# Kernel tuning notes

Measured on AMD Instinct MI355X. Metric: run time of the kernel, lower is better.

## Reference

```python
import jax, jax.numpy as jnp
import numpy as np

P = 16  # patch size
D = 768  # embedding dim


def setup_inputs() -> dict:
    key = jax.random.key(0)
    k_img, k_w, k_b = jax.random.split(key, 3)
    B, H, W, C = 64, 224, 224, 3
    image = jax.random.normal(k_img, (B, H, W, C), dtype=jnp.float32)
    patch_dim = P * P * C  # 768
    # Keras Dense default: glorot_uniform kernel, zeros bias
    limit = np.sqrt(6.0 / (patch_dim + D)).astype(np.float32)
    W_proj = jax.random.uniform(k_w, (patch_dim, D), dtype=jnp.float32,
                                minval=-limit, maxval=limit)
    b_proj = jnp.zeros((D,), dtype=jnp.float32)
    return {"image": image, "W_proj": W_proj, "b_proj": b_proj}


def reference(image, W_proj, b_proj):
    B, H, W, C = image.shape
    nh, nw = H // P, W // P
    # Fused im2col replacing the per-patch slicing loop:
    # [B,H,W,C] -> [B, nh, P, nw, P, C] -> [B, nh, nw, P, P, C] -> [B, nh*nw, P*P*C]
    # Row-major (p_i, p_j) patch order matches the original nested loop, and
    # flatten of a [B,P,P,C] slice matches the (P,P,C) raveling here.
    patches = image.reshape(B, nh, P, nw, P, C)
    patches = patches.transpose(0, 1, 3, 2, 4, 5).reshape(B, nh * nw, P * P * C)
    # Dense + exact GELU (tf.keras.activations.gelu default approximate=False)
    x = jnp.einsum('bnp,pd->bnd', patches, W_proj) + b_proj
    return jax.nn.gelu(x, approximate=False)
```

## Files before the change

kernel.cpp:

```cpp
#include <hip/hip_runtime.h>
#include <hip/hip_bf16.h>
#include <math.h>

#define MM 12544
#define KK 768
#define NN 768
#define BM 64
#define BN 256
#define BK 64
#define KT 12
#define MT 196
#define NT 3
#define TILE_B_BYTES (BN*BK*2)

#define WTPACK_BLOCKS ((NN * 96) / 256)

typedef __bf16 v8bf __attribute__((ext_vector_type(8)));
typedef float  v4f  __attribute__((ext_vector_type(4)));

__global__ __launch_bounds__(256) void wpack_kernel(const float* __restrict__ w,
                                                    __hip_bfloat16* __restrict__ wpack) {
    int tid = blockIdx.x * 256 + threadIdx.x;
    int n   = tid % 768;
    int gg  = tid / 768;
    int k0  = gg * 8;
    float f[8];
#pragma unroll
    for (int j = 0; j < 8; j++) f[j] = w[(size_t)(k0 + j) * NN + n];
    int nt = n >> 8;
    int nr = n & 255;
    int kt = gg >> 3;
    int g  = gg & 7;
    int gs = g ^ (nr & 7);
    union { __hip_bfloat16 h[8]; uint4 u; } o;
#pragma unroll
    for (int j = 0; j < 8; j++) o.h[j] = __float2bfloat16(f[j]);
    *(uint4*)(wpack + ((size_t)(nt * KT + kt) * BN + nr) * BK + gs * 8) = o.u;
}

__device__ __forceinline__ float gelu_fast(float x) {
    float t2 = 1.5957691216057308f * x * (1.0f + 0.044715f * x * x);
    float e  = __expf(t2);
    float r  = __builtin_amdgcn_rcpf(e + 1.0f);
    return x - x * r;
}

__global__ __launch_bounds__(256, 3) void gemm_fused(const float* __restrict__ img,
                                                     const __hip_bfloat16* __restrict__ wpack,
                                                     const float* __restrict__ bias,
                                                     float* __restrict__ out) {
    __shared__ __align__(16) __hip_bfloat16 As[BM * BK];
    __shared__ __align__(16) __hip_bfloat16 Bs[BN * BK];

    const int blk = blockIdx.x;
    const int nt  = blk % 3;
    const int mt  = blk / 3;

    const int tid  = threadIdx.x;
    const int lane = tid & 63;
    const int wave = tid >> 6;
    const int wn   = wave * 64;
    const int col  = lane & 15;
    const int quad = lane >> 4;
    const int cl7  = col & 7;

    const int r  = tid >> 2;
    const int c  = tid & 3;
    const int m  = mt * BM + r;
    const int b  = m / 196;
    const int pm = m - b * 196;
    const int pr = pm / 14;
    const int pc = pm - pr * 14;
    const float* abase = img + (size_t)((b * 224 + pr * 16) * 224 + pc * 16) * 3;
    int rem = (c == 3) ? 0 : c * 16;
    const float* asrc = abase + ((c == 3) ? 672 : 0) + rem;
    const int s0 = (2 * c) ^ (r & 7);
    uint4* aw0 = (uint4*)(As + r * BK + s0 * 8);
    uint4* aw1 = (uint4*)(As + r * BK + (s0 ^ 1) * 8);

    v4f acc[4][4];
    const v4f vzero = {0.f, 0.f, 0.f, 0.f};
#pragma unroll
    for (int a = 0; a < 4; a++)
#pragma unroll
        for (int cc = 0; cc < 4; cc++) acc[a][cc] = vzero;

    const char* bT = (const char*)wpack + (size_t)nt * KT * TILE_B_BYTES;

    float4 a0, a1, a2, a3;
    {
        const float4* ap = (const float4*)asrc;
        a0 = ap[0]; a1 = ap[1]; a2 = ap[2]; a3 = ap[3];
        asrc += (rem < 32) ? 688 : 1312;
        rem   = (rem < 32) ? rem + 16 : 0;
    }

    for (int kt = 0; kt < KT; kt++) {
#pragma unroll
        for (int p = 0; p < 8; p++) {
            int off = p * 4096 + tid * 16;
            __builtin_amdgcn_global_load_lds(
                (const __attribute__((address_space(1))) void*)(bT + off),
                (__attribute__((address_space(3))) void*)((char*)Bs + off), 16, 0, 0);
        }
        bT += TILE_B_BYTES;

        union { __hip_bfloat16 h[8]; uint4 u; } o0, o1;
        o0.h[0] = __float2bfloat16(a0.x); o0.h[1] = __float2bfloat16(a0.y);
        o0.h[2] = __float2bfloat16(a0.z); o0.h[3] = __float2bfloat16(a0.w);
        o0.h[4] = __float2bfloat16(a1.x); o0.h[5] = __float2bfloat16(a1.y);
        o0.h[6] = __float2bfloat16(a1.z); o0.h[7] = __float2bfloat16(a1.w);
        o1.h[0] = __float2bfloat16(a2.x); o1.h[1] = __float2bfloat16(a2.y);
        o1.h[2] = __float2bfloat16(a2.z); o1.h[3] = __float2bfloat16(a2.w);
        o1.h[4] = __float2bfloat16(a3.x); o1.h[5] = __float2bfloat16(a3.y);
        o1.h[6] = __float2bfloat16(a3.z); o1.h[7] = __float2bfloat16(a3.w);
        *aw0 = o0.u;
        *aw1 = o1.u;

        if (kt + 1 < KT) {
            const float4* ap = (const float4*)asrc;
            a0 = ap[0]; a1 = ap[1]; a2 = ap[2]; a3 = ap[3];
            asrc += (rem < 32) ? 688 : 1312;
            rem   = (rem < 32) ? rem + 16 : 0;
        }
        __syncthreads();

#pragma unroll
        for (int ks = 0; ks < 2; ks++) {
            const int gs = (ks * 4 + quad) ^ cl7;
            const v8bf* pa = (const v8bf*)(As + col * BK + gs * 8);
            const v8bf* pb = (const v8bf*)(Bs + (wn + col) * BK + gs * 8);
            v8bf af[4], bfr[4];
#pragma unroll
            for (int mi = 0; mi < 4; mi++) af[mi] = pa[mi * 128];
#pragma unroll
            for (int ni = 0; ni < 4; ni++) bfr[ni] = pb[ni * 128];
#pragma unroll
            for (int mi = 0; mi < 4; mi++)
#pragma unroll
                for (int ni = 0; ni < 4; ni++)
                    acc[mi][ni] = __builtin_amdgcn_mfma_f32_16x16x32_bf16(
                        af[mi], bfr[ni], acc[mi][ni], 0, 0, 0);
        }
        __syncthreads();
    }

#pragma unroll
    for (int ni = 0; ni < 4; ni++) {
        int n    = nt * BN + wn + ni * 16 + col;
        float bv = bias[n];
#pragma unroll
        for (int mi = 0; mi < 4; mi++) {
            int rowb = mt * BM + mi * 16 + quad * 4;
            float* po = out + (size_t)rowb * NN + n;
#pragma unroll
            for (int rg = 0; rg < 4; rg++) {
                float x = acc[mi][ni][rg] + bv;
                po[(size_t)rg * NN] = gelu_fast(x);
            }
        }
    }
}

extern "C" void kernel_launch(void* const* d_in, const int* in_sizes, int n_in,
                              void* d_out, int out_size, void* d_ws, size_t ws_size,
                              hipStream_t stream) {
    const float* img   = (const float*)d_in[0];
    const float* wproj = (const float*)d_in[1];
    const float* bias  = (const float*)d_in[2];
    float* out = (float*)d_out;

    __hip_bfloat16* wpack = (__hip_bfloat16*)d_ws;

    wpack_kernel<<<dim3(WTPACK_BLOCKS), dim3(256), 0, stream>>>(wproj, wpack);
    gemm_fused<<<dim3(MT * NT), dim3(256), 0, stream>>>(img, wpack, bias, out);
}
```

Measured before the change: 123.4 us.

## Double-buffer LDS tiles and remap blocks per XCD for L2 locality

```diff
diff --git a/kernel.cpp b/kernel.cpp
--- a/kernel.cpp
+++ b/kernel.cpp
@@ -45,16 +45,19 @@
     return x - x * r;
 }
 
-__global__ __launch_bounds__(256, 3) void gemm_fused(const float* __restrict__ img,
+__global__ __launch_bounds__(256, 2) void gemm_fused(const float* __restrict__ img,
                                                      const __hip_bfloat16* __restrict__ wpack,
                                                      const float* __restrict__ bias,
                                                      float* __restrict__ out) {
-    __shared__ __align__(16) __hip_bfloat16 As[BM * BK];
-    __shared__ __align__(16) __hip_bfloat16 Bs[BN * BK];
+    __shared__ __align__(16) __hip_bfloat16 As[2][BM * BK];
+    __shared__ __align__(16) __hip_bfloat16 Bs[2][BN * BK];
 
-    const int blk = blockIdx.x;
-    const int nt  = blk % 3;
-    const int mt  = blk / 3;
+    const int h   = blockIdx.x;
+    const int xcd = h & 7;
+    const int j   = h >> 3;
+    const int u   = (xcd < 4 ? xcd * 74 : 296 + (xcd - 4) * 73) + j;
+    const int nt  = u % 3;
+    const int mt  = u / 3;
 
     const int tid  = threadIdx.x;
     const int lane = tid & 63;
@@ -74,9 +77,9 @@
     const float* abase = img + (size_t)((b * 224 + pr * 16) * 224 + pc * 16) * 3;
     int rem = (c == 3) ? 0 : c * 16;
     const float* asrc = abase + ((c == 3) ? 672 : 0) + rem;
-    const int s0 = (2 * c) ^ (r & 7);
-    uint4* aw0 = (uint4*)(As + r * BK + s0 * 8);
-    uint4* aw1 = (uint4*)(As + r * BK + (s0 ^ 1) * 8);
+    const int s0   = (2 * c) ^ (r & 7);
+    const int aoff0 = r * BK + s0 * 8;
+    const int aoff1 = r * BK + (s0 ^ 1) * 8;
 
     v4f acc[4][4];
     const v4f vzero = {0.f, 0.f, 0.f, 0.f};
@@ -87,63 +90,72 @@
 
     const char* bT = (const char*)wpack + (size_t)nt * KT * TILE_B_BYTES;
 
+#define LOAD_A_REGS()                                            \
+    {   const float4* ap = (const float4*)asrc;                  \
+        a0 = ap[0]; a1 = ap[1]; a2 = ap[2]; a3 = ap[3];          \
+        asrc += (rem < 32) ? 688 : 1312;                         \
+        rem   = (rem < 32) ? rem + 16 : 0;  }
+
+#define STAGE_B(buf)                                                          \
+    {   _Pragma("unroll")                                                     \
+        for (int p = 0; p < 8; p++) {                                         \
+            int off = p * 4096 + tid * 16;                                    \
+            __builtin_amdgcn_global_load_lds(                                 \
+                (const __attribute__((address_space(1))) void*)(bT + off),    \
+                (__attribute__((address_space(3))) void*)((char*)Bs[buf] + off), \
+                16, 0, 0);                                                    \
+        }                                                                     \
+        bT += TILE_B_BYTES;  }
+
+#define WRITE_A(buf)                                                          \
+    {   union { __hip_bfloat16 hh[8]; uint4 uu; } o0, o1;                     \
+        o0.hh[0] = __float2bfloat16(a0.x); o0.hh[1] = __float2bfloat16(a0.y); \
+        o0.hh[2] = __float2bfloat16(a0.z); o0.hh[3] = __float2bfloat16(a0.w); \
+        o0.hh[4] = __float2bfloat16(a1.x); o0.hh[5] = __float2bfloat16(a1.y); \
+        o0.hh[6] = __float2bfloat16(a1.z); o0.hh[7] = __float2bfloat16(a1.w); \
+        o1.hh[0] = __float2bfloat16(a2.x); o1.hh[1] = __float2bfloat16(a2.y); \
+        o1.hh[2] = __float2bfloat16(a2.z); o1.hh[3] = __float2bfloat16(a2.w); \
+        o1.hh[4] = __float2bfloat16(a3.x); o1.hh[5] = __float2bfloat16(a3.y); \
+        o1.hh[6] = __float2bfloat16(a3.z); o1.hh[7] = __float2bfloat16(a3.w); \
+        *(uint4*)(As[buf] + aoff0) = o0.uu;                                   \
+        *(uint4*)(As[buf] + aoff1) = o1.uu;  }
+
+#define COMPUTE(buf)                                                          \
+    {   _Pragma("unroll")                                                     \
+        for (int ks = 0; ks < 2; ks++) {                                      \
+            const int gs = (ks * 4 + quad) ^ cl7;                             \
+            const v8bf* pa = (const v8bf*)(As[buf] + col * BK + gs * 8);      \
+            const v8bf* pb = (const v8bf*)(Bs[buf] + (wn + col) * BK + gs * 8);\
+            v8bf af[4], bfr[4];                                               \
+            _Pragma("unroll")                                                 \
+            for (int mi = 0; mi < 4; mi++) af[mi] = pa[mi * 128];             \
+            _Pragma("unroll")                                                 \
+            for (int ni = 0; ni < 4; ni++) bfr[ni] = pb[ni * 128];            \
+            _Pragma("unroll")                                                 \
+            for (int mi = 0; mi < 4; mi++)                                    \
+                _Pragma("unroll")                                             \
+                for (int ni = 0; ni < 4; ni++)                                \
+                    acc[mi][ni] = __builtin_amdgcn_mfma_f32_16x16x32_bf16(    \
+                        af[mi], bfr[ni], acc[mi][ni], 0, 0, 0);               \
+        }  }
+
     float4 a0, a1, a2, a3;
-    {
-        const float4* ap = (const float4*)asrc;
-        a0 = ap[0]; a1 = ap[1]; a2 = ap[2]; a3 = ap[3];
-        asrc += (rem < 32) ? 688 : 1312;
-        rem   = (rem < 32) ? rem + 16 : 0;
-    }
-
-    for (int kt = 0; kt < KT; kt++) {
-#pragma unroll
-        for (int p = 0; p < 8; p++) {
-            int off = p * 4096 + tid * 16;
-            __builtin_amdgcn_global_load_lds(
-                (const __attribute__((address_space(1))) void*)(bT + off),
-                (__attribute__((address_space(3))) void*)((char*)Bs + off), 16, 0, 0);
-        }
-        bT += TILE_B_BYTES;
-
-        union { __hip_bfloat16 h[8]; uint4 u; } o0, o1;
-        o0.h[0] = __float2bfloat16(a0.x); o0.h[1] = __float2bfloat16(a0.y);
-        o0.h[2] = __float2bfloat16(a0.z); o0.h[3] = __float2bfloat16(a0.w);
-        o0.h[4] = __float2bfloat16(a1.x); o0.h[5] = __float2bfloat16(a1.y);
-        o0.h[6] = __float2bfloat16(a1.z); o0.h[7] = __float2bfloat16(a1.w);
-        o1.h[0] = __float2bfloat16(a2.x); o1.h[1] = __float2bfloat16(a2.y);
-        o1.h[2] = __float2bfloat16(a2.z); o1.h[3] = __float2bfloat16(a2.w);
-        o1.h[4] = __float2bfloat16(a3.x); o1.h[5] = __float2bfloat16(a3.y);
-        o1.h[6] = __float2bfloat16(a3.z); o1.h[7] = __float2bfloat16(a3.w);
-        *aw0 = o0.u;
-        *aw1 = o1.u;
-
-        if (kt + 1 < KT) {
-            const float4* ap = (const float4*)asrc;
-            a0 = ap[0]; a1 = ap[1]; a2 = ap[2]; a3 = ap[3];
-            asrc += (rem < 32) ? 688 : 1312;
-            rem   = (rem < 32) ? rem + 16 : 0;
-        }
-        __syncthreads();
+    LOAD_A_REGS();
+    STAGE_B(0);
+    WRITE_A(0);
+    LOAD_A_REGS();
+    __syncthreads();
 
 #pragma unroll
-        for (int ks = 0; ks < 2; ks++) {
-            const int gs = (ks * 4 + quad) ^ cl7;
-            const v8bf* pa = (const v8bf*)(As + col * BK + gs * 8);
-            const v8bf* pb = (const v8bf*)(Bs + (wn + col) * BK + gs * 8);
-            v8bf af[4], bfr[4];
-#pragma unroll
-            for (int mi = 0; mi < 4; mi++) af[mi] = pa[mi * 128];
-#pragma unroll
-            for (int ni = 0; ni < 4; ni++) bfr[ni] = pb[ni * 128];
-#pragma unroll
-            for (int mi = 0; mi < 4; mi++)
-#pragma unroll
-                for (int ni = 0; ni < 4; ni++)
-                    acc[mi][ni] = __builtin_amdgcn_mfma_f32_16x16x32_bf16(
-                        af[mi], bfr[ni], acc[mi][ni], 0, 0, 0);
-        }
+    for (int t = 0; t < KT - 1; t++) {
+        const int cur = t & 1;
+        STAGE_B(cur ^ 1);
+        WRITE_A(cur ^ 1);
+        if (t < KT - 2) LOAD_A_REGS();
+        COMPUTE(cur);
         __syncthreads();
     }
+    COMPUTE((KT - 1) & 1);
 
 #pragma unroll
     for (int ni = 0; ni < 4; ni++) {
@@ -160,6 +172,10 @@
             }
         }
     }
+#undef LOAD_A_REGS
+#undef STAGE_B
+#undef WRITE_A
+#undef COMPUTE
 }
 
 extern "C" void kernel_launch(void* const* d_in, const int* in_sizes, int n_in,
```

Measured after the change: 126.9 us. 2.8% more time.
